# Performance work log

Measured on AMD Instinct MI355X. Metric: run time of the kernel, lower is better.

The kernel has to match this reference:

```python
import jax, jax.numpy as jnp
import numpy as np

GROUP = 4
SG = 4          # shared_gp
C = 256         # inchannels
N = 1024
BS = 16         # GROUP * batch
EPS = 1e-6


def _ln(x, g, b):
    # torch LayerNorm over last dim, biased variance, eps=1e-6
    mu = jnp.mean(x, axis=-1, keepdims=True)
    var = jnp.var(x, axis=-1, keepdims=True)
    return (x - mu) / jnp.sqrt(var + EPS) * g + b


def setup_inputs() -> dict:
    key = jax.random.key(0)
    ks = jax.random.split(key, 12)
    cg = C // SG
    s_conv = 1.0 / np.sqrt(cg)
    s_full = 1.0 / np.sqrt(C)
    return {
        "x": jax.random.normal(ks[0], (BS, C, N), jnp.float32),
        # grouped 1x1 convs (bias=False): weight (SG, C/SG out, C/SG in)
        "Wq": jax.random.normal(ks[1], (SG, cg, cg), jnp.float32) * s_conv,
        "Wk": jax.random.normal(ks[2], (SG, cg, cg), jnp.float32) * s_conv,
        # v conv: full 1x1 conv with bias
        "Wv": jax.random.normal(ks[3], (C, C), jnp.float32) * s_full,
        "bv": jax.random.normal(ks[4], (C,), jnp.float32) * 0.01,
        "ln1_g": jnp.ones((C,), jnp.float32),
        "ln1_b": jnp.zeros((C,), jnp.float32),
        "W1": jax.random.normal(ks[5], (4 * C, C), jnp.float32) * s_full,
        "b1": jax.random.normal(ks[6], (4 * C,), jnp.float32) * 0.01,
        "W2": jax.random.normal(ks[7], (C, 4 * C), jnp.float32) * (1.0 / np.sqrt(4 * C)),
        "b2": jax.random.normal(ks[8], (C,), jnp.float32) * 0.01,
        "ln2_g": jnp.ones((C,), jnp.float32),
        "ln2_b": jnp.zeros((C,), jnp.float32),
    }


def reference(x, Wq, Wk, Wv, bv, ln1_g, ln1_b, W1, b1, W2, b2, ln2_g, ln2_b):
    bs, ch, n = x.shape
    group, sg = GROUP, SG
    b = bs // group
    cg = ch // sg
    first = x[:b]          # (b, C, N)
    last = x[b:]           # ((g-1)*b, C, N)

    # grouped 1x1 convs: y[.,g,o,n] = sum_i W[g,o,i] * x[.,g,i,n]
    xq = jnp.einsum('goi,Bgin->Bgon', Wq, last.reshape((group - 1) * b, sg, cg, n))
    xq = xq.reshape(group - 1, b, sg, cg, n)              # (g-1, b, sg, cg, N)
    xk = jnp.einsum('goi,bgin->bgon', Wk, first.reshape(b, sg, cg, n))  # (b, sg, cg, N)
    xv = jnp.einsum('oc,bcn->bon', Wv, first) + bv[None, :, None]        # (b, C, N)

    # energy: q^T k per shared group, summed over shared groups -> (g-1, b, N, N)
    energy = jnp.einsum('gbscn,bscm->gbnm', xq, xk)
    attn = jax.nn.softmax(energy, axis=-1)
    # x_r[g,b,c,m] = sum_n v[b,c,n] attn[g,b,n,m], scaled by 1/sqrt(C)
    x_r = jnp.einsum('bcn,gbnm->gbcm', xv, attn) / jnp.sqrt(jnp.float32(ch))

    # faithful to torch: vstack (group-major) then view(batch, group-1, ...).mean(1)
    x_r = x_r.reshape(b, group - 1, ch, n).mean(axis=1)   # (b, C, N)

    h = _ln((first + x_r).transpose(0, 2, 1), ln1_g, ln1_b)  # (b, N, C)
    h = h + jax.nn.relu(h @ W1.T + b1) @ W2.T + b2
    h = jax.nn.relu(_ln(h, ln2_g, ln2_b))
    out_first = h.transpose(0, 2, 1)                       # (b, C, N)
    return jnp.concatenate([out_first, last], axis=0)
```

## Files before the change

kernel.cpp:

```cpp
#include <hip/hip_runtime.h>

#define CC 256
#define NN 1024
#define CN (CC*NN)

typedef __attribute__((ext_vector_type(8))) short short8;
typedef __attribute__((ext_vector_type(8))) unsigned short u16x8;
typedef __attribute__((ext_vector_type(4))) float f32x4;

__device__ __forceinline__ unsigned short f2bf(float x) {
  unsigned u = __float_as_uint(x);
  u = u + 0x7fffu + ((u >> 16) & 1u);
  return (unsigned short)(u >> 16);
}
__device__ __forceinline__ float bf2f(unsigned short b) {
  return __uint_as_float(((unsigned)b) << 16);
}
__device__ __forceinline__ void gload_lds16(const unsigned short* g, unsigned short* l) {
  __builtin_amdgcn_global_load_lds(
      (const __attribute__((address_space(1))) unsigned short*)g,
      (__attribute__((address_space(3))) unsigned short*)l, 16, 0, 0);
}

__global__ __launch_bounds__(256) void prep_kernel(
    const float* __restrict__ x, const float* __restrict__ Wq,
    const float* __restrict__ Wk, const float* __restrict__ Wv,
    const float* __restrict__ bv,
    const float4* __restrict__ W1, const float4* __restrict__ W2,
    unsigned short* __restrict__ w1_bf, unsigned short* __restrict__ w2_bf,
    unsigned short* __restrict__ xT, unsigned short* __restrict__ xqT,
    unsigned short* __restrict__ xkT, unsigned short* __restrict__ xv_bf,
    float* __restrict__ out) {
  __shared__ float shbuf[64 * 133];
  int bz = blockIdx.x, t = threadIdx.x;
  if (bz < 512) {
    int id = bz * 256 + t;
    const float4* s; unsigned short* d; int k;
    if (id < 65536) { s = W1; d = w1_bf; k = id; }
    else            { s = W2; d = w2_bf; k = id - 65536; }
    float4 v = s[k];
    ushort4 o; o.x = f2bf(v.x); o.y = f2bf(v.y); o.z = f2bf(v.z); o.w = f2bf(v.w);
    *(ushort4*)&d[k * 4] = o;
  } else if (bz < 768) {
    float (*tile)[65] = (float(*)[65])shbuf;
    int zz = bz - 512;
    int b = zz >> 6, c0 = ((zz >> 4) & 3) * 64, n0 = (zz & 15) * 64;
    int tr = t >> 6, tc = t & 63;
#pragma unroll
    for (int r = 0; r < 16; ++r) {
      int c = tr + r * 4;
      tile[c][tc] = x[(long)b * CN + (long)(c0 + c) * NN + n0 + tc];
    }
    __syncthreads();
#pragma unroll
    for (int r = 0; r < 16; ++r) {
      int n = tr + r * 4;
      xT[(long)b * CN + (long)(n0 + n) * CC + c0 + tc] = f2bf(tile[tc][n]);
    }
  } else if (bz < 1792) {
    float (*xs)[68] = (float(*)[68])shbuf;
    float (*Ws)[65] = (float(*)[65])(shbuf + 64 * 68);
    int zz = bz - 768;
    int z = zz >> 6, g = (zz >> 4) & 3, n0 = (zz & 15) * 64;
    const float* src; const float* W; unsigned short* dst;
    if (z < 12) { src = x + (long)(4 + z) * CN; W = Wq; dst = xqT + (long)z * CN; }
    else        { src = x + (long)(z - 12) * CN; W = Wk; dst = xkT + (long)(z - 12) * CN; }
    int tr = t >> 6, tc = t & 63;
#pragma unroll
    for (int r = 0; r < 16; ++r) {
      int i = tr + r * 4;
      xs[i][tc] = src[(long)(g * 64 + i) * NN + n0 + tc];
      Ws[i][tc] = W[(g * 64 + i) * 64 + tc];
    }
    __syncthreads();
    int o = tc, q = tr;
    float acc[16];
#pragma unroll
    for (int k = 0; k < 16; ++k) acc[k] = 0.f;
    for (int i = 0; i < 64; ++i) {
      float w = Ws[o][i];
      const float4* xr4 = (const float4*)&xs[i][q * 16];
#pragma unroll
      for (int k = 0; k < 4; ++k) {
        float4 v = xr4[k];
        acc[4*k+0] += w * v.x; acc[4*k+1] += w * v.y;
        acc[4*k+2] += w * v.z; acc[4*k+3] += w * v.w;
      }
    }
#pragma unroll
    for (int k = 0; k < 16; ++k)
      dst[(long)(n0 + q * 16 + k) * CC + g * 64 + o] = f2bf(acc[k]);
  } else if (bz < 2048) {
    float (*xs)[68] = (float(*)[68])shbuf;
    float (*Ws)[65] = (float(*)[65])(shbuf + 64 * 68);
    int zz = bz - 1792;
    int b = zz >> 6, o0 = ((zz >> 4) & 3) * 64, n0 = (zz & 15) * 64;
    int tr = t >> 6, tc = t & 63;
    float acc[16];
#pragma unroll
    for (int k = 0; k < 16; ++k) acc[k] = 0.f;
    for (int cb = 0; cb < 4; ++cb) {
      __syncthreads();
#pragma unroll
      for (int r = 0; r < 16; ++r) {
        int i = tr + r * 4;
        xs[i][tc] = x[(long)b * CN + (long)(cb * 64 + i) * NN + n0 + tc];
        Ws[i][tc] = Wv[(long)(o0 + i) * 256 + cb * 64 + tc];
      }
      __syncthreads();
      for (int i = 0; i < 64; ++i) {
        float w = Ws[tc][i];
        const float4* xr4 = (const float4*)&xs[i][tr * 16];
#pragma unroll
        for (int k = 0; k < 4; ++k) {
          float4 v = xr4[k];
          acc[4*k+0] += w * v.x; acc[4*k+1] += w * v.y;
          acc[4*k+2] += w * v.z; acc[4*k+3] += w * v.w;
        }
      }
    }
    float bvv = bv[o0 + tc];
#pragma unroll
    for (int k = 0; k < 16; ++k)
      xv_bf[((long)b * CC + o0 + tc) * NN + n0 + tr * 16 + k] = f2bf(acc[k] + bvv);
  } else {
    int zz = bz - 2048;
    const float4* src = (const float4*)(x + 4L * CN);
    float4* dst = (float4*)(out + 4L * CN);
#pragma unroll
    for (int k = 0; k < 4; ++k) {
      int idx = zz * 1024 + k * 256 + t;
      dst[idx] = src[idx];
    }
  }
}

template<int BIASROW, int BIASCOL, int RELU, int OUTBF, int STATS>
__global__ __launch_bounds__(256) void mgemm(
    const unsigned short* __restrict__ A, const unsigned short* __restrict__ B,
    void* __restrict__ Cout, const float* __restrict__ bias,
    float2* __restrict__ part,
    int lda, int ldb, int ldc, int K,
    long sA, int amod, long sB, int bmod, long sC, float alpha) {
  __shared__ unsigned short As[128 * 32];
  __shared__ unsigned short Bs[128 * 32];
  int z = blockIdx.z;
  A += (long)(z % amod) * sA;
  B += (long)(z % bmod) * sB;
  int t = threadIdx.x, w = t >> 6, l = t & 63;
  int wr = w >> 1, wc = w & 1;
  long i0 = blockIdx.y * 128, j0 = blockIdx.x * 128;
  f32x4 acc[4][4];
#pragma unroll
  for (int a = 0; a < 4; ++a)
#pragma unroll
    for (int b = 0; b < 4; ++b) acc[a][b] = (f32x4){0.f, 0.f, 0.f, 0.f};
  int lr = l & 15, lk = (l >> 4) * 8;
  for (int k0 = 0; k0 < K; k0 += 32) {
#pragma unroll
    for (int it = 0; it < 2; ++it) {
      int chunk = t + it * 256;
      int row = chunk >> 2, kq = chunk & 3;
      gload_lds16(A + (i0 + row) * (long)lda + k0 + kq * 8, &As[chunk * 8]);
      gload_lds16(B + (j0 + row) * (long)ldb + k0 + kq * 8, &Bs[chunk * 8]);
    }
    __syncthreads();
    short8 af[4], bfr[4];
#pragma unroll
    for (int f = 0; f < 4; ++f) af[f]  = *(const short8*)&As[(wr * 64 + f * 16 + lr) * 32 + lk];
#pragma unroll
    for (int f = 0; f < 4; ++f) bfr[f] = *(const short8*)&Bs[(wc * 64 + f * 16 + lr) * 32 + lk];
#pragma unroll
    for (int fm = 0; fm < 4; ++fm)
#pragma unroll
      for (int fn = 0; fn < 4; ++fn)
        acc[fm][fn] = __builtin_amdgcn_mfma_f32_16x16x32_bf16(af[fm], bfr[fn], acc[fm][fn], 0, 0, 0);
    __syncthreads();
  }
  long cz = (long)z * sC;
  int li = (l >> 4) * 4, lj = l & 15;
#pragma unroll
  for (int fm = 0; fm < 4; ++fm)
#pragma unroll
    for (int fn = 0; fn < 4; ++fn) {
      long ib = i0 + wr * 64 + fm * 16 + li;
      long j  = j0 + wc * 64 + fn * 16 + lj;
#pragma unroll
      for (int r = 0; r < 4; ++r) {
        long i = ib + r;
        float v = acc[fm][fn][r] * alpha;
        if (BIASCOL) v += bias[j];
        if (BIASROW) v += bias[i];
        if (RELU)    v = fmaxf(v, 0.f);
        if (OUTBF) ((unsigned short*)Cout)[cz + i * ldc + j] = f2bf(v);
        else       ((float*)Cout)[cz + i * ldc + j] = v;
      }
    }
  if (STATS) {
    int chunk = blockIdx.y * 2 + wr;
#pragma unroll
    for (int fn = 0; fn < 4; ++fn) {
      float mx = -1e30f;
#pragma unroll
      for (int fm = 0; fm < 4; ++fm)
#pragma unroll
        for (int r = 0; r < 4; ++r) mx = fmaxf(mx, acc[fm][fn][r]);
      mx = fmaxf(mx, __shfl_xor(mx, 16));
      mx = fmaxf(mx, __shfl_xor(mx, 32));
      float sm = 0.f;
#pragma unroll
      for (int fm = 0; fm < 4; ++fm)
#pragma unroll
        for (int r = 0; r < 4; ++r) sm += __expf(acc[fm][fn][r] - mx);
      sm += __shfl_xor(sm, 16);
      sm += __shfl_xor(sm, 32);
      if (l < 16) {
        long n = j0 + wc * 64 + fn * 16 + l;
        part[((long)z * 16 + chunk) * NN + n] = make_float2(mx, sm);
      }
    }
  }
}

__global__ __launch_bounds__(256) void pv_gemm(
    const unsigned short* __restrict__ E, const unsigned short* __restrict__ XV,
    const float2* __restrict__ part, unsigned short* __restrict__ xrp) {
  __shared__ unsigned short As[128 * 32];
  __shared__ unsigned short Bs[128 * 32];
  __shared__ float Ms[256];
  __shared__ float Ds[256];
  int z = blockIdx.z;
  int q = z >> 2, s = z & 3;
  const unsigned short* A = E + (long)q * NN * NN + s * 256;
  const unsigned short* B = XV + (long)(q & 3) * CN + s * 256;
  int t = threadIdx.x;
  {
    int n = s * 256 + t;
    float mx = -1e30f;
#pragma unroll
    for (int c = 0; c < 16; ++c) mx = fmaxf(mx, part[((long)q * 16 + c) * NN + n].x);
    float sm = 0.f;
#pragma unroll
    for (int c = 0; c < 16; ++c) {
      float2 p = part[((long)q * 16 + c) * NN + n];
      sm += p.y * __expf(p.x - mx);
    }
    Ms[t] = mx;
    Ds[t] = 1.f / sm;
  }
  int w = t >> 6, l = t & 63;
  int wr = w >> 1, wc = w & 1;
  long i0 = blockIdx.y * 128, j0 = blockIdx.x * 128;
  f32x4 acc[4][4];
#pragma unroll
  for (int a = 0; a < 4; ++a)
#pragma unroll
    for (int b = 0; b < 4; ++b) acc[a][b] = (f32x4){0.f, 0.f, 0.f, 0.f};
  int lr = l & 15, lk = (l >> 4) * 8;
  int ar = t >> 1, ah = (t & 1) * 16;
  __syncthreads();
  for (int k0 = 0; k0 < 256; k0 += 32) {
#pragma unroll
    for (int it = 0; it < 2; ++it) {
      int chunk = t + it * 256;
      int row = chunk >> 2, kq = chunk & 3;
      gload_lds16(B + (j0 + row) * 1024L + k0 + kq * 8, &Bs[chunk * 8]);
    }
    u16x8 e0 = *(const u16x8*)&A[(i0 + ar) * 1024L + k0 + ah];
    u16x8 e1 = *(const u16x8*)&A[(i0 + ar) * 1024L + k0 + ah + 8];
    u16x8 p0, p1;
#pragma unroll
    for (int j = 0; j < 8; ++j) {
      int n = k0 + ah + j;
      p0[j] = f2bf(__expf(bf2f(e0[j]) - Ms[n]) * Ds[n]);
    }
#pragma unroll
    for (int j = 0; j < 8; ++j) {
      int n = k0 + ah + 8 + j;
      p1[j] = f2bf(__expf(bf2f(e1[j]) - Ms[n]) * Ds[n]);
    }
    *(u16x8*)&As[ar * 32 + ah]     = p0;
    *(u16x8*)&As[ar * 32 + ah + 8] = p1;
    __syncthreads();
    short8 af[4], bfr[4];
#pragma unroll
    for (int f = 0; f < 4; ++f) af[f]  = *(const short8*)&As[(wr * 64 + f * 16 + lr) * 32 + lk];
#pragma unroll
    for (int f = 0; f < 4; ++f) bfr[f] = *(const short8*)&Bs[(wc * 64 + f * 16 + lr) * 32 + lk];
#pragma unroll
    for (int fm = 0; fm < 4; ++fm)
#pragma unroll
      for (int fn = 0; fn < 4; ++fn)
        acc[fm][fn] = __builtin_amdgcn_mfma_f32_16x16x32_bf16(af[fm], bfr[fn], acc[fm][fn], 0, 0, 0);
    __syncthreads();
  }
  long cz = (long)(s * 12 + q) << 18;
  int li = (l >> 4) * 4, lj = l & 15;
#pragma unroll
  for (int fm = 0; fm < 4; ++fm)
#pragma unroll
    for (int fn = 0; fn < 4; ++fn) {
      long ib = i0 + wr * 64 + fm * 16 + li;
      long j  = j0 + wc * 64 + fn * 16 + lj;
#pragma unroll
      for (int r = 0; r < 4; ++r)
        xrp[cz + (ib + r) * 256 + j] = f2bf(acc[fm][fn][r] * (1.f / 16.f));
    }
}

__global__ __launch_bounds__(256) void mix_ln1(
    const unsigned short* __restrict__ xT, const unsigned short* __restrict__ xrp,
    const float* __restrict__ g, const float* __restrict__ bb,
    unsigned short* __restrict__ h_bf) {
  __shared__ float r1[4], r2[4];
  int bn = blockIdx.x;
  int i = bn >> 10, n = bn & 1023;
  int c = threadIdx.x;
  long no = (long)n * CC + c;
  float a = 0.f;
#pragma unroll
  for (int j = 0; j < 3; ++j)
#pragma unroll
    for (int s = 0; s < 4; ++s)
      a += bf2f(xrp[((long)(s * 12 + 3 * i + j) << 18) + no]);
  float v = bf2f(xT[(long)i * CN + no]) + a * (1.f / 3.f);
  float sS = v, s2 = v * v;
#pragma unroll
  for (int m = 32; m; m >>= 1) { sS += __shfl_xor(sS, m); s2 += __shfl_xor(s2, m); }
  if ((c & 63) == 0) { r1[c >> 6] = sS; r2[c >> 6] = s2; }
  __syncthreads();
  float mu = (r1[0] + r1[1] + r1[2] + r1[3]) * (1.f / 256.f);
  float var = (r2[0] + r2[1] + r2[2] + r2[3]) * (1.f / 256.f) - mu * mu;
  float o = (v - mu) * rsqrtf(var + 1e-6f) * g[c] + bb[c];
  h_bf[(long)bn * CC + c] = f2bf(o);
}

__global__ __launch_bounds__(256) void ln2t(
    const unsigned short* __restrict__ pm, const unsigned short* __restrict__ h_bf,
    const float* __restrict__ b2, const float* __restrict__ g,
    const float* __restrict__ bb, float* __restrict__ out) {
  __shared__ float tile[16][261];
  __shared__ float smu[16], srs[16];
  int i = blockIdx.y, n0 = blockIdx.x * 16;
  int t = threadIdx.x;
  float bc = b2[t];
#pragma unroll
  for (int r = 0; r < 16; ++r) {
    long row = (long)i * NN + n0 + r;
    float v = bc + bf2f(h_bf[row * CC + t]);
#pragma unroll
    for (int s = 0; s < 4; ++s) v += bf2f(pm[((long)s << 20) + row * CC + t]);
    tile[r][t] = v;
  }
  __syncthreads();
  int w = t >> 6, l = t & 63;
#pragma unroll
  for (int rr = 0; rr < 4; ++rr) {
    int r = w * 4 + rr;
    float s = 0.f, s2 = 0.f;
#pragma unroll
    for (int k = 0; k < 4; ++k) { float v = tile[r][l + 64 * k]; s += v; s2 += v * v; }
#pragma unroll
    for (int m = 32; m; m >>= 1) { s += __shfl_xor(s, m); s2 += __shfl_xor(s2, m); }
    if (l == 0) {
      float mu = s * (1.f / 256.f);
      float var = s2 * (1.f / 256.f) - mu * mu;
      smu[r] = mu; srs[r] = rsqrtf(var + 1e-6f);
    }
  }
  __syncthreads();
#pragma unroll
  for (int k = 0; k < 16; ++k) {
    int nn = t & 15, c = (t >> 4) + 16 * k;
    float v = (tile[nn][c] - smu[nn]) * srs[nn] * g[c] + bb[c];
    out[((long)i * CC + c) * NN + n0 + nn] = fmaxf(v, 0.f);
  }
}

extern "C" void kernel_launch(void* const* d_in, const int* in_sizes, int n_in,
                              void* d_out, int out_size, void* d_ws, size_t ws_size,
                              hipStream_t stream) {
  const float* x   = (const float*)d_in[0];
  const float* Wq  = (const float*)d_in[1];
  const float* Wk  = (const float*)d_in[2];
  const float* Wv  = (const float*)d_in[3];
  const float* bv  = (const float*)d_in[4];
  const float* g1  = (const float*)d_in[5];
  const float* b1v = (const float*)d_in[6];
  const float* W1  = (const float*)d_in[7];
  const float* b1m = (const float*)d_in[8];
  const float* W2  = (const float*)d_in[9];
  const float* b2m = (const float*)d_in[10];
  const float* g2  = (const float*)d_in[11];
  const float* b2v = (const float*)d_in[12];
  float* out = (float*)d_out;

  char* base = (char*)d_ws;
  unsigned short* E_bf   = (unsigned short*)base;
  unsigned short* h_bf   = (unsigned short*)base;
  unsigned short* hid_bf = (unsigned short*)(base + (2u << 20));
  size_t off = 24u << 20;
  unsigned short* xrp    = (unsigned short*)(base + off); off += 25165824;
  unsigned short* p_mlp  = (unsigned short*)(base + off); off += 8388608;
  unsigned short* w1_bf  = (unsigned short*)(base + off); off += 524288;
  unsigned short* w2_bf  = (unsigned short*)(base + off); off += 524288;
  unsigned short* xt_bf  = (unsigned short*)(base + off); off += 2097152;
  unsigned short* xqt_bf = (unsigned short*)(base + off); off += 6291456;
  unsigned short* xkt_bf = (unsigned short*)(base + off); off += 2097152;
  unsigned short* xv_bf  = (unsigned short*)(base + off); off += 2097152;
  float2* part           = (float2*)(base + off);         off += 1572864;

  prep_kernel<<<2816, 256, 0, stream>>>(x, Wq, Wk, Wv, bv,
      (const float4*)W1, (const float4*)W2, w1_bf, w2_bf,
      xt_bf, xqt_bf, xkt_bf, xv_bf, out);
  mgemm<0,0,0,1,1><<<dim3(8, 8, 12), 256, 0, stream>>>(
      xkt_bf, xqt_bf, E_bf, nullptr, part,
      256, 256, 1024, 256, (long)CN, 4, (long)CN, 12, (long)NN * NN, 1.f);
  pv_gemm<<<dim3(2, 8, 48), 256, 0, stream>>>(E_bf, xv_bf, part, xrp);
  mix_ln1<<<4096, 256, 0, stream>>>(xt_bf, xrp, g1, b1v, h_bf);
  mgemm<0,1,1,1,0><<<dim3(8, 32, 1), 256, 0, stream>>>(
      h_bf, w1_bf, hid_bf, b1m, nullptr,
      256, 256, 1024, 256, 0L, 1, 0L, 1, 0L, 1.f);
  mgemm<0,0,0,1,0><<<dim3(2, 32, 4), 256, 0, stream>>>(
      hid_bf, w2_bf, p_mlp, nullptr, nullptr,
      1024, 1024, 256, 256, 256L, 4, 256L, 4, 1048576L, 1.f);
  ln2t<<<dim3(64, 4), 256, 0, stream>>>(p_mlp, h_bf, b2m, g2, b2v, out);
}
```

Baseline: 200.6 us.

## Move V projection to MFMA GEMM fused with energy GEMM launch

The V projection (Wv·x + bias) moves off the scalar FP32 LDS-tiled path in the prep kernel. Wv is now converted to bf16 in prep and the projection runs as extra MFMA tiles inside a new attn_gemm kernel, which also computes the energy GEMM with its softmax partial stats. The q/k grouped conv tiles in prep shrink to 32 columns so more blocks run in parallel, and the output copy is moved to the front of prep. The trade-off is some extra bf16 rounding on the V path and a mixed-role kernel whose V-projection blocks are in the same grid as the energy tiles.

```diff
diff --git a/kernel.cpp b/kernel.cpp
--- a/kernel.cpp
+++ b/kernel.cpp
@@ -24,26 +24,34 @@
 
 __global__ __launch_bounds__(256) void prep_kernel(
     const float* __restrict__ x, const float* __restrict__ Wq,
-    const float* __restrict__ Wk, const float* __restrict__ Wv,
-    const float* __restrict__ bv,
+    const float* __restrict__ Wk, const float4* __restrict__ Wv,
     const float4* __restrict__ W1, const float4* __restrict__ W2,
+    unsigned short* __restrict__ wv_bf,
     unsigned short* __restrict__ w1_bf, unsigned short* __restrict__ w2_bf,
     unsigned short* __restrict__ xT, unsigned short* __restrict__ xqT,
-    unsigned short* __restrict__ xkT, unsigned short* __restrict__ xv_bf,
-    float* __restrict__ out) {
-  __shared__ float shbuf[64 * 133];
+    unsigned short* __restrict__ xkT, float* __restrict__ out) {
+  __shared__ float shbuf[6464];
   int bz = blockIdx.x, t = threadIdx.x;
-  if (bz < 512) {
-    int id = bz * 256 + t;
+  if (bz < 768) {
+    const float4* src = (const float4*)(x + 4L * CN);
+    float4* dst = (float4*)(out + 4L * CN);
+#pragma unroll
+    for (int k = 0; k < 4; ++k) {
+      int idx = bz * 1024 + k * 256 + t;
+      dst[idx] = src[idx];
+    }
+  } else if (bz < 1344) {
+    int id = (bz - 768) * 256 + t;
     const float4* s; unsigned short* d; int k;
-    if (id < 65536) { s = W1; d = w1_bf; k = id; }
-    else            { s = W2; d = w2_bf; k = id - 65536; }
+    if (id < 16384)      { s = Wv; d = wv_bf; k = id; }
+    else if (id < 81920) { s = W1; d = w1_bf; k = id - 16384; }
+    else                 { s = W2; d = w2_bf; k = id - 81920; }
     float4 v = s[k];
     ushort4 o; o.x = f2bf(v.x); o.y = f2bf(v.y); o.z = f2bf(v.z); o.w = f2bf(v.w);
     *(ushort4*)&d[k * 4] = o;
-  } else if (bz < 768) {
+  } else if (bz < 1600) {
     float (*tile)[65] = (float(*)[65])shbuf;
-    int zz = bz - 512;
+    int zz = bz - 1344;
     int b = zz >> 6, c0 = ((zz >> 4) & 3) * 64, n0 = (zz & 15) * 64;
     int tr = t >> 6, tc = t & 63;
 #pragma unroll
@@ -57,11 +65,11 @@
       int n = tr + r * 4;
       xT[(long)b * CN + (long)(n0 + n) * CC + c0 + tc] = f2bf(tile[tc][n]);
     }
-  } else if (bz < 1792) {
-    float (*xs)[68] = (float(*)[68])shbuf;
-    float (*Ws)[65] = (float(*)[65])(shbuf + 64 * 68);
-    int zz = bz - 768;
-    int z = zz >> 6, g = (zz >> 4) & 3, n0 = (zz & 15) * 64;
+  } else {
+    float (*Ws)[65] = (float(*)[65])shbuf;
+    float (*xs)[36] = (float(*)[36])(shbuf + 64 * 65);
+    int zz = bz - 1600;
+    int z = zz >> 7, g = (zz >> 5) & 3, n0 = (zz & 31) * 32;
     const float* src; const float* W; unsigned short* dst;
     if (z < 12) { src = x + (long)(4 + z) * CN; W = Wq; dst = xqT + (long)z * CN; }
     else        { src = x + (long)(z - 12) * CN; W = Wk; dst = xkT + (long)(z - 12) * CN; }
@@ -69,79 +77,130 @@
 #pragma unroll
     for (int r = 0; r < 16; ++r) {
       int i = tr + r * 4;
-      xs[i][tc] = src[(long)(g * 64 + i) * NN + n0 + tc];
       Ws[i][tc] = W[(g * 64 + i) * 64 + tc];
     }
-    __syncthreads();
-    int o = tc, q = tr;
-    float acc[16];
-#pragma unroll
-    for (int k = 0; k < 16; ++k) acc[k] = 0.f;
+#pragma unroll
+    for (int r = 0; r < 8; ++r) {
+      int i = r * 8 + (t >> 5);
+      xs[i][t & 31] = src[(long)(g * 64 + i) * NN + n0 + (t & 31)];
+    }
+    __syncthreads();
+    int o = tc, qd = tr;
+    float acc[8];
+#pragma unroll
+    for (int k = 0; k < 8; ++k) acc[k] = 0.f;
     for (int i = 0; i < 64; ++i) {
       float w = Ws[o][i];
-      const float4* xr4 = (const float4*)&xs[i][q * 16];
-#pragma unroll
-      for (int k = 0; k < 4; ++k) {
-        float4 v = xr4[k];
-        acc[4*k+0] += w * v.x; acc[4*k+1] += w * v.y;
-        acc[4*k+2] += w * v.z; acc[4*k+3] += w * v.w;
+      const float4* xr4 = (const float4*)&xs[i][qd * 8];
+      float4 a0 = xr4[0], a1 = xr4[1];
+      acc[0] += w * a0.x; acc[1] += w * a0.y; acc[2] += w * a0.z; acc[3] += w * a0.w;
+      acc[4] += w * a1.x; acc[5] += w * a1.y; acc[6] += w * a1.z; acc[7] += w * a1.w;
+    }
+#pragma unroll
+    for (int k = 0; k < 8; ++k)
+      dst[(long)(n0 + qd * 8 + k) * CC + g * 64 + o] = f2bf(acc[k]);
+  }
+}
+
+__global__ __launch_bounds__(256) void attn_gemm(
+    const unsigned short* __restrict__ xkt, const unsigned short* __restrict__ xqt,
+    const unsigned short* __restrict__ wv, const unsigned short* __restrict__ xt,
+    const float* __restrict__ bv, unsigned short* __restrict__ E,
+    unsigned short* __restrict__ xv, float2* __restrict__ part) {
+  __shared__ unsigned short As[128 * 32];
+  __shared__ unsigned short Bs[128 * 32];
+  int z = blockIdx.x;
+  const unsigned short *A, *B;
+  unsigned short* Co;
+  long i0, j0;
+  int q = 0;
+  bool isXV = z < 64;
+  if (isXV) {
+    int b = z >> 4, r = z & 15;
+    i0 = (r >> 3) * 128; j0 = (r & 7) * 128;
+    A = wv; B = xt + (long)b * CN; Co = xv + (long)b * CN;
+  } else {
+    int ze = z - 64;
+    q = ze >> 6; int r = ze & 63;
+    i0 = (r >> 3) * 128; j0 = (r & 7) * 128;
+    A = xkt + (long)(q & 3) * CN; B = xqt + (long)q * CN;
+    Co = E + (long)q * NN * NN;
+  }
+  int t = threadIdx.x, w = t >> 6, l = t & 63;
+  int wr = w >> 1, wc = w & 1;
+  f32x4 acc[4][4];
+#pragma unroll
+  for (int a = 0; a < 4; ++a)
+#pragma unroll
+    for (int b = 0; b < 4; ++b) acc[a][b] = (f32x4){0.f, 0.f, 0.f, 0.f};
+  int lr = l & 15, lk = (l >> 4) * 8;
+  for (int k0 = 0; k0 < 256; k0 += 32) {
+#pragma unroll
+    for (int it = 0; it < 2; ++it) {
+      int chunk = t + it * 256;
+      int row = chunk >> 2, kq = chunk & 3;
+      gload_lds16(A + (i0 + row) * 256L + k0 + kq * 8, &As[chunk * 8]);
+      gload_lds16(B + (j0 + row) * 256L + k0 + kq * 8, &Bs[chunk * 8]);
+    }
+    __syncthreads();
+    short8 af[4], bfr[4];
+#pragma unroll
+    for (int f = 0; f < 4; ++f) af[f]  = *(const short8*)&As[(wr * 64 + f * 16 + lr) * 32 + lk];
+#pragma unroll
+    for (int f = 0; f < 4; ++f) bfr[f] = *(const short8*)&Bs[(wc * 64 + f * 16 + lr) * 32 + lk];
+#pragma unroll
+    for (int fm = 0; fm < 4; ++fm)
+#pragma unroll
+      for (int fn = 0; fn < 4; ++fn)
+        acc[fm][fn] = __builtin_amdgcn_mfma_f32_16x16x32_bf16(af[fm], bfr[fn], acc[fm][fn], 0, 0, 0);
+    __syncthreads();
+  }
+  int li = (l >> 4) * 4, lj = l & 15;
+#pragma unroll
+  for (int fm = 0; fm < 4; ++fm)
+#pragma unroll
+    for (int fn = 0; fn < 4; ++fn) {
+      long ib = i0 + wr * 64 + fm * 16 + li;
+      long j  = j0 + wc * 64 + fn * 16 + lj;
+#pragma unroll
+      for (int r = 0; r < 4; ++r) {
+        float v = acc[fm][fn][r];
+        if (isXV) v += bv[ib + r];
+        Co[(ib + r) * 1024 + j] = f2bf(v);
       }
     }
-#pragma unroll
-    for (int k = 0; k < 16; ++k)
-      dst[(long)(n0 + q * 16 + k) * CC + g * 64 + o] = f2bf(acc[k]);
-  } else if (bz < 2048) {
-    float (*xs)[68] = (float(*)[68])shbuf;
-    float (*Ws)[65] = (float(*)[65])(shbuf + 64 * 68);
-    int zz = bz - 1792;
-    int b = zz >> 6, o0 = ((zz >> 4) & 3) * 64, n0 = (zz & 15) * 64;
-    int tr = t >> 6, tc = t & 63;
-    float acc[16];
-#pragma unroll
-    for (int k = 0; k < 16; ++k) acc[k] = 0.f;
-    for (int cb = 0; cb < 4; ++cb) {
-      __syncthreads();
-#pragma unroll
-      for (int r = 0; r < 16; ++r) {
-        int i = tr + r * 4;
-        xs[i][tc] = x[(long)b * CN + (long)(cb * 64 + i) * NN + n0 + tc];
-        Ws[i][tc] = Wv[(long)(o0 + i) * 256 + cb * 64 + tc];
+  if (!isXV) {
+    int chunk = (int)(i0 >> 6) + wr;
+#pragma unroll
+    for (int fn = 0; fn < 4; ++fn) {
+      float mx = -1e30f;
+#pragma unroll
+      for (int fm = 0; fm < 4; ++fm)
+#pragma unroll
+        for (int r = 0; r < 4; ++r) mx = fmaxf(mx, acc[fm][fn][r]);
+      mx = fmaxf(mx, __shfl_xor(mx, 16));
+      mx = fmaxf(mx, __shfl_xor(mx, 32));
+      float sm = 0.f;
+#pragma unroll
+      for (int fm = 0; fm < 4; ++fm)
+#pragma unroll
+        for (int r = 0; r < 4; ++r) sm += __expf(acc[fm][fn][r] - mx);
+      sm += __shfl_xor(sm, 16);
+      sm += __shfl_xor(sm, 32);
+      if (l < 16) {
+        long n = j0 + wc * 64 + fn * 16 + l;
+        part[((long)q * 16 + chunk) * NN + n] = make_float2(mx, sm);
       }
-      __syncthreads();
-      for (int i = 0; i < 64; ++i) {
-        float w = Ws[tc][i];
-        const float4* xr4 = (const float4*)&xs[i][tr * 16];
-#pragma unroll
-        for (int k = 0; k < 4; ++k) {
-          float4 v = xr4[k];
-          acc[4*k+0] += w * v.x; acc[4*k+1] += w * v.y;
-          acc[4*k+2] += w * v.z; acc[4*k+3] += w * v.w;
-        }
-      }
-    }
-    float bvv = bv[o0 + tc];
-#pragma unroll
-    for (int k = 0; k < 16; ++k)
-      xv_bf[((long)b * CC + o0 + tc) * NN + n0 + tr * 16 + k] = f2bf(acc[k] + bvv);
-  } else {
-    int zz = bz - 2048;
-    const float4* src = (const float4*)(x + 4L * CN);
-    float4* dst = (float4*)(out + 4L * CN);
-#pragma unroll
-    for (int k = 0; k < 4; ++k) {
-      int idx = zz * 1024 + k * 256 + t;
-      dst[idx] = src[idx];
-    }
-  }
-}
-
-template<int BIASROW, int BIASCOL, int RELU, int OUTBF, int STATS>
+    }
+  }
+}
+
+template<int BIASCOL, int RELU>
 __global__ __launch_bounds__(256) void mgemm(
     const unsigned short* __restrict__ A, const unsigned short* __restrict__ B,
-    void* __restrict__ Cout, const float* __restrict__ bias,
-    float2* __restrict__ part,
+    unsigned short* __restrict__ Cout, const float* __restrict__ bias,
     int lda, int ldb, int ldc, int K,
-    long sA, int amod, long sB, int bmod, long sC, float alpha) {
+    long sA, int amod, long sB, int bmod, long sC) {
   __shared__ unsigned short As[128 * 32];
   __shared__ unsigned short Bs[128 * 32];
   int z = blockIdx.z;
@@ -187,39 +246,12 @@
       long j  = j0 + wc * 64 + fn * 16 + lj;
 #pragma unroll
       for (int r = 0; r < 4; ++r) {
-        long i = ib + r;
-        float v = acc[fm][fn][r] * alpha;
+        float v = acc[fm][fn][r];
         if (BIASCOL) v += bias[j];
-        if (BIASROW) v += bias[i];
         if (RELU)    v = fmaxf(v, 0.f);
-        if (OUTBF) ((unsigned short*)Cout)[cz + i * ldc + j] = f2bf(v);
-        else       ((float*)Cout)[cz + i * ldc + j] = v;
+        Cout[cz + (ib + r) * ldc + j] = f2bf(v);
       }
     }
-  if (STATS) {
-    int chunk = blockIdx.y * 2 + wr;
-#pragma unroll
-    for (int fn = 0; fn < 4; ++fn) {
-      float mx = -1e30f;
-#pragma unroll
-      for (int fm = 0; fm < 4; ++fm)
-#pragma unroll
-        for (int r = 0; r < 4; ++r) mx = fmaxf(mx, acc[fm][fn][r]);
-      mx = fmaxf(mx, __shfl_xor(mx, 16));
-      mx = fmaxf(mx, __shfl_xor(mx, 32));
-      float sm = 0.f;
-#pragma unroll
-      for (int fm = 0; fm < 4; ++fm)
-#pragma unroll
-        for (int r = 0; r < 4; ++r) sm += __expf(acc[fm][fn][r] - mx);
-      sm += __shfl_xor(sm, 16);
-      sm += __shfl_xor(sm, 32);
-      if (l < 16) {
-        long n = j0 + wc * 64 + fn * 16 + l;
-        part[((long)z * 16 + chunk) * NN + n] = make_float2(mx, sm);
-      }
-    }
-  }
 }
 
 __global__ __launch_bounds__(256) void pv_gemm(
@@ -402,6 +434,7 @@
   size_t off = 24u << 20;
   unsigned short* xrp    = (unsigned short*)(base + off); off += 25165824;
   unsigned short* p_mlp  = (unsigned short*)(base + off); off += 8388608;
+  unsigned short* wv_bf  = (unsigned short*)(base + off); off += 131072;
   unsigned short* w1_bf  = (unsigned short*)(base + off); off += 524288;
   unsigned short* w2_bf  = (unsigned short*)(base + off); off += 524288;
   unsigned short* xt_bf  = (unsigned short*)(base + off); off += 2097152;
@@ -410,19 +443,18 @@
   unsigned short* xv_bf  = (unsigned short*)(base + off); off += 2097152;
   float2* part           = (float2*)(base + off);         off += 1572864;
 
-  prep_kernel<<<2816, 256, 0, stream>>>(x, Wq, Wk, Wv, bv,
-      (const float4*)W1, (const float4*)W2, w1_bf, w2_bf,
-      xt_bf, xqt_bf, xkt_bf, xv_bf, out);
-  mgemm<0,0,0,1,1><<<dim3(8, 8, 12), 256, 0, stream>>>(
-      xkt_bf, xqt_bf, E_bf, nullptr, part,
-      256, 256, 1024, 256, (long)CN, 4, (long)CN, 12, (long)NN * NN, 1.f);
+  prep_kernel<<<3648, 256, 0, stream>>>(x, Wq, Wk, (const float4*)Wv,
+      (const float4*)W1, (const float4*)W2, wv_bf, w1_bf, w2_bf,
+      xt_bf, xqt_bf, xkt_bf, out);
+  attn_gemm<<<832, 256, 0, stream>>>(xkt_bf, xqt_bf, wv_bf, xt_bf,
+      bv, E_bf, xv_bf, part);
   pv_gemm<<<dim3(2, 8, 48), 256, 0, stream>>>(E_bf, xv_bf, part, xrp);
   mix_ln1<<<4096, 256, 0, stream>>>(xt_bf, xrp, g1, b1v, h_bf);
-  mgemm<0,1,1,1,0><<<dim3(8, 32, 1), 256, 0, stream>>>(
-      h_bf, w1_bf, hid_bf, b1m, nullptr,
-      256, 256, 1024, 256, 0L, 1, 0L, 1, 0L, 1.f);
-  mgemm<0,0,0,1,0><<<dim3(2, 32, 4), 256, 0, stream>>>(
-      hid_bf, w2_bf, p_mlp, nullptr, nullptr,
-      1024, 1024, 256, 256, 256L, 4, 256L, 4, 1048576L, 1.f);
+  mgemm<1,1><<<dim3(8, 32, 1), 256, 0, stream>>>(
+      h_bf, w1_bf, hid_bf, b1m,
+      256, 256, 1024, 256, 0L, 1, 0L, 1, 0L);
+  mgemm<0,0><<<dim3(2, 32, 4), 256, 0, stream>>>(
+      hid_bf, w2_bf, p_mlp, nullptr,
+      1024, 1024, 256, 256, 256L, 4, 256L, 4, 1048576L);
   ln2t<<<dim3(64, 4), 256, 0, stream>>>(p_mlp, h_bf, b2m, g2, b2v, out);
 }
```

New measurement: 178.2 us. -11.2%, faster.
